# Kernel tuning notes

Measured on AMD Instinct MI355X. Metric: run time of the kernel, lower is better.

The kernel has to match this reference:

```python
import jax, jax.numpy as jnp
import numpy as np

# Batched-graph geometry: 128 graphs x 400 nodes x 6400 edges
N_GRAPHS = 128
NODES_PER = 400
EDGES_PER = 6400
N_NODES = N_GRAPHS * NODES_PER      # 51200
N_EDGES = N_GRAPHS * EDGES_PER      # 819200
F_IN = 256
HID = 64
K = 8          # num_filtrations
D = 3          # outputs per coordinate function (4 funs -> 12 total)


def coord_feats(p, t_tri, t_gau, sig, W_lin, b_lin, c_rh, r_rh):
    """Apply the 4 coordinate transforms to persistence pairs p: [K, M, 2].
    Returns [M, K*4D] with layout cat-over-coordfuns inside, cat-over-filtrations outside,
    matching torch: cat([cat([mod(p_k) for mod in funs],1) for k],1)."""
    x0, x1 = p[..., 0:1], p[..., 1:2]                       # [K,M,1]
    tri = jax.nn.relu(x1 - jnp.abs(t_tri - x0))             # Triangle_transform -> [K,M,D]
    d2 = jnp.sum((p[..., None, :] - t_gau) ** 2, axis=-1)   # [K,M,D]
    gau = jnp.exp(-d2 / (2.0 * sig[0] ** 2))                # Gaussian_transform
    lin = p @ W_lin + b_lin                                 # Line_transform
    l1 = jnp.abs(x0 - c_rh) + jnp.abs(x1 - c_rh)            # L1 dist to centers
    rh = 1.0 / (1.0 + l1) - 1.0 / (1.0 + jnp.abs(jnp.abs(r_rh[0]) - l1))  # RationalHat
    feats = jnp.concatenate([tri, gau, lin, rh], axis=-1)   # [K,M,4D]
    Kk, M, Dd = feats.shape
    return feats.transpose(1, 0, 2).reshape(M, Kk * Dd)     # [M, K*4D]


def setup_inputs() -> dict:
    key = jax.random.key(0)
    ks = jax.random.split(key, 24)
    x = jax.random.normal(ks[0], (N_NODES, F_IN), jnp.float32)
    # edges drawn within each graph block
    offs = (jnp.arange(N_EDGES) // EDGES_PER) * NODES_PER
    edge_index = jax.random.randint(ks[1], (2, N_EDGES), 0, NODES_PER) + offs[None, :]
    batch_vec = jnp.arange(N_NODES) // NODES_PER            # graph id per node
    edge_slices = jnp.arange(N_GRAPHS + 1) * EDGES_PER
    s = lambda i, shape: (jax.random.normal(ks[i], shape, jnp.float32) * 0.1)
    inp = dict(
        x=x, edge_index=edge_index, batch_vec=batch_vec, edge_slices=edge_slices,
        # shared filtration MLP: Linear(F_IN,HID)-ReLU-Linear(HID,K)-ReLU
        W1=s(2, (F_IN, HID)), b1=jnp.zeros((HID,), jnp.float32),
        W2=s(3, (HID, K)), b2=jnp.zeros((K,), jnp.float32),
        # dim-0 coordinate-function params
        t_tri0=s(4, (D,)), t_gau0=s(5, (D, 2)), sig0=jnp.ones((1,), jnp.float32),
        W_lin0=s(6, (2, D)), b_lin0=jnp.zeros((D,), jnp.float32),
        c_rh0=s(7, (D,)), r_rh0=jnp.ones((1,), jnp.float32),
        # dim-1 coordinate-function params
        t_tri1=s(8, (D,)), t_gau1=s(9, (D, 2)), sig1=jnp.ones((1,), jnp.float32),
        W_lin1=s(10, (2, D)), b_lin1=jnp.zeros((D,), jnp.float32),
        c_rh1=s(11, (D,)), r_rh1=jnp.ones((1,), jnp.float32),
        # output linear: in = F_IN + 2*K*4D (dist_dim1=True, non-residual path)
        W_out=s(12, (F_IN + 2 * K * 4 * D, F_IN)), b_out=jnp.zeros((F_IN,), jnp.float32),
    )
    return inp


def reference(x, edge_index, batch_vec, edge_slices,
              W1, b1, W2, b2,
              t_tri0, t_gau0, sig0, W_lin0, b_lin0, c_rh0, r_rh0,
              t_tri1, t_gau1, sig1, W_lin1, b_lin1, c_rh1, r_rh1,
              W_out, b_out):
    # per-node filtration values (shared params, relu_filtrations)
    fv = jax.nn.relu(jax.nn.relu(x @ W1 + b1) @ W2 + b2)            # [N,K]
    # edge filtration = max of endpoint values
    fe = jnp.maximum(fv[edge_index[0]], fv[edge_index[1]])          # [E,K]
    # fake dim-0 persistence: pairs (v, v) for every vertex, per filtration
    pers0 = jnp.broadcast_to(fv.T[..., None], (K, fv.shape[0], 2))  # [K,N,2]
    # fake dim-1: one unpaired tuple per graph = max edge value, placed at first edge
    eb = batch_vec[edge_index[0]]                                   # [E] graph id per edge
    unpaired = jax.ops.segment_max(fe, eb, num_segments=N_GRAPHS)   # [B,K]
    chosen = edge_slices[:-1]                                       # deterministic edge per graph
    pers1 = jnp.zeros((edge_index.shape[1], K, 2), fv.dtype)
    pers1 = pers1.at[chosen, :, 0].set(unpaired)
    pers1 = pers1.transpose(1, 0, 2)                                # [K,E,2]
    # coordinate-function activations
    act0 = coord_feats(pers0, t_tri0, t_gau0, sig0, W_lin0, b_lin0, c_rh0, r_rh0)  # [N, K*12]
    mask = jnp.any(pers1 != 0, axis=(0, 2))                         # [E]
    act1 = coord_feats(pers1, t_tri1, t_gau1, sig1, W_lin1, b_lin1, c_rh1, r_rh1)  # [E, K*12]
    g1 = jax.ops.segment_sum(act1 * mask[:, None].astype(act1.dtype), eb,
                             num_segments=N_GRAPHS)                 # [B, K*12]
    concat = jnp.concatenate([x, act0, g1[batch_vec]], axis=1)      # [N, F_IN + 2*K*12]
    return jax.nn.relu(concat @ W_out + b_out)                      # [N, F_IN]
```

## Files before the change

kernel.cpp:

```cpp
#include <hip/hip_runtime.h>
#include <hip/hip_bf16.h>

#define N_GRAPHS 128
#define NODES_PER 400
#define EDGES_PER 6400
#define N_NODES (N_GRAPHS * NODES_PER)
#define N_EDGES (N_GRAPHS * EDGES_PER)
#define F_IN 256
#define HID 64
#define FEAT 96
#define KTOT 352

typedef __attribute__((ext_vector_type(8))) short bf16x8;
typedef __attribute__((ext_vector_type(4))) float f32x4;

union u4b8 { uint4 u; bf16x8 v; };

__device__ __forceinline__ unsigned short f2b(float f) {
  union { float f; unsigned int u; } c; c.f = f;
  const unsigned int r = c.u + 0x7FFFu + ((c.u >> 16) & 1u);
  return (unsigned short)(r >> 16);
}

__device__ __forceinline__ unsigned pkbf2(float lo, float hi) {
  __hip_bfloat162 h = __float22bfloat162_rn(make_float2(lo, hi));
  return *reinterpret_cast<unsigned*>(&h);
}

__device__ __forceinline__ float coord_one(
    int fun, int d, float x0, float x1,
    const float* __restrict__ t_tri, const float* __restrict__ t_gau,
    const float* __restrict__ sig, const float* __restrict__ W_lin,
    const float* __restrict__ b_lin, const float* __restrict__ c_rh,
    const float* __restrict__ r_rh) {
  if (fun == 0) {
    return fmaxf(x1 - fabsf(t_tri[d] - x0), 0.f);
  } else if (fun == 1) {
    const float dx = x0 - t_gau[d * 2 + 0];
    const float dy = x1 - t_gau[d * 2 + 1];
    const float s = sig[0];
    return expf(-(dx * dx + dy * dy) / (2.f * s * s));
  } else if (fun == 2) {
    return x0 * W_lin[d] + x1 * W_lin[3 + d] + b_lin[d];
  } else {
    const float l1 = fabsf(x0 - c_rh[d]) + fabsf(x1 - c_rh[d]);
    return 1.f / (1.f + l1) - 1.f / (1.f + fabsf(fabsf(r_rh[0]) - l1));
  }
}

__global__ __launch_bounds__(256) void k_wt(
    const float* __restrict__ W_out, const float* __restrict__ W1,
    unsigned short* __restrict__ Wt2, unsigned short* __restrict__ Wt1c) {
  const int idx = blockIdx.x * 256 + threadIdx.x;
  if (idx < KTOT * 256) {
    const int k = idx >> 8, c = idx & 255;
    Wt2[((size_t)(k >> 3) * 256 + c) * 8 + (k & 7)] = f2b(W_out[idx]);
  } else {
    const int j = idx - KTOT * 256;
    const int k = j >> 6, c = j & 63;
    Wt1c[((size_t)(k >> 3) * 64 + c) * 8 + (k & 7)] = f2b(W1[j]);
  }
}

__global__ __launch_bounds__(256, 3) void k_fv(
    const float* __restrict__ x, const unsigned short* __restrict__ Wt1c,
    const float* __restrict__ b1, const float* __restrict__ W2,
    const float* __restrict__ b2,
    const float* __restrict__ t_tri, const float* __restrict__ t_gau,
    const float* __restrict__ sig, const float* __restrict__ W_lin,
    const float* __restrict__ b_lin, const float* __restrict__ c_rh,
    const float* __restrict__ r_rh,
    float* __restrict__ fv, unsigned short* __restrict__ ext,
    unsigned short* __restrict__ xb, const int write_xb) {
  __shared__ float W2s[HID * 8];
  __shared__ float Hs[4][16][68];
  const int tid = threadIdx.x;
  const int wave = tid >> 6, lane = tid & 63;
  const int l15 = lane & 15, l4 = lane >> 4;
  const int n0 = blockIdx.x * 64;

  W2s[tid] = W2[tid];
  W2s[tid + 256] = W2[tid + 256];
  __syncthreads();

  const int arow = n0 + wave * 16 + l15;
  bf16x8 afr[8];
  #pragma unroll
  for (int kt = 0; kt < 8; ++kt) {
    const size_t go = (size_t)arow * F_IN + kt * 32 + l4 * 8;
    const float4 f0 = *(const float4*)&x[go];
    const float4 f1 = *(const float4*)&x[go + 4];
    u4b8 w;
    w.u.x = pkbf2(f0.x, f0.y);
    w.u.y = pkbf2(f0.z, f0.w);
    w.u.z = pkbf2(f1.x, f1.y);
    w.u.w = pkbf2(f1.z, f1.w);
    if (write_xb) *(uint4*)&xb[go] = w.u;
    afr[kt] = w.v;
  }

  f32x4 acc[4];
  #pragma unroll
  for (int nf = 0; nf < 4; ++nf) acc[nf] = (f32x4){0.f, 0.f, 0.f, 0.f};
  #pragma unroll
  for (int kt = 0; kt < 8; ++kt) {
    const unsigned short* wb = Wt1c + (size_t)(kt * 4 + l4) * 512;
    #pragma unroll
    for (int nf = 0; nf < 4; ++nf) {
      const bf16x8 b = *(const bf16x8*)&wb[(nf * 16 + l15) * 8];
      acc[nf] = __builtin_amdgcn_mfma_f32_16x16x32_bf16(afr[kt], b, acc[nf], 0, 0, 0);
    }
  }

  #pragma unroll
  for (int nf = 0; nf < 4; ++nf) {
    const int col = nf * 16 + l15;
    const float bb = b1[col];
    #pragma unroll
    for (int j = 0; j < 4; ++j)
      Hs[wave][l4 * 4 + j][col] = fmaxf(acc[nf][j] + bb, 0.f);
  }
  __syncthreads();

  #pragma unroll
  for (int p = tid; p < 512; p += 256) {
    const int row = p >> 3, kk = p & 7;
    const float* hr = Hs[row >> 4][row & 15];
    float s = b2[kk];
    #pragma unroll 8
    for (int j = 0; j < HID; ++j) s = fmaf(hr[j], W2s[j * 8 + kk], s);
    s = fmaxf(s, 0.f);
    const int n = n0 + row;
    fv[(size_t)n * 8 + kk] = s;

    float fo[12];
    #pragma unroll
    for (int fun = 0; fun < 4; ++fun)
      #pragma unroll
      for (int d = 0; d < 3; ++d)
        fo[fun * 3 + d] = coord_one(fun, d, s, s,
                                    t_tri, t_gau, sig, W_lin, b_lin, c_rh, r_rh);
    unsigned o32[6];
    #pragma unroll
    for (int i = 0; i < 6; ++i) o32[i] = pkbf2(fo[2 * i], fo[2 * i + 1]);
    unsigned short* dst = &ext[(size_t)n * FEAT + kk * 12];
    *(uint2*)&dst[0] = make_uint2(o32[0], o32[1]);
    *(uint2*)&dst[4] = make_uint2(o32[2], o32[3]);
    *(uint2*)&dst[8] = make_uint2(o32[4], o32[5]);
  }
}

#define CHUNK (EDGES_PER / 8)
__global__ __launch_bounds__(256) void k_unpaired(
    const int* __restrict__ ei, const float* __restrict__ fv,
    float* __restrict__ unpP) {
  __shared__ float lfv[NODES_PER * 8];
  __shared__ float red[256][8];
  const int g = blockIdx.x >> 3, ch = blockIdx.x & 7;
  const int tid = threadIdx.x;

  for (int i = tid; i < NODES_PER * 2; i += 256)
    *(float4*)&lfv[i * 4] = *(const float4*)&fv[(size_t)g * NODES_PER * 8 + i * 4];
  __syncthreads();

  float lm[8];
  #pragma unroll
  for (int k = 0; k < 8; ++k) lm[k] = 0.f;
  const int e0 = g * EDGES_PER + ch * CHUNK;
  for (int e = e0 + tid; e < e0 + CHUNK; e += 256) {
    const int a = ei[e] - g * NODES_PER;
    const int b = ei[N_EDGES + e] - g * NODES_PER;
    const float4 a0 = *(const float4*)&lfv[a * 8];
    const float4 a1 = *(const float4*)&lfv[a * 8 + 4];
    const float4 b0 = *(const float4*)&lfv[b * 8];
    const float4 b1 = *(const float4*)&lfv[b * 8 + 4];
    lm[0] = fmaxf(lm[0], fmaxf(a0.x, b0.x));
    lm[1] = fmaxf(lm[1], fmaxf(a0.y, b0.y));
    lm[2] = fmaxf(lm[2], fmaxf(a0.z, b0.z));
    lm[3] = fmaxf(lm[3], fmaxf(a0.w, b0.w));
    lm[4] = fmaxf(lm[4], fmaxf(a1.x, b1.x));
    lm[5] = fmaxf(lm[5], fmaxf(a1.y, b1.y));
    lm[6] = fmaxf(lm[6], fmaxf(a1.z, b1.z));
    lm[7] = fmaxf(lm[7], fmaxf(a1.w, b1.w));
  }
  #pragma unroll
  for (int k = 0; k < 8; ++k) red[tid][k] = lm[k];
  __syncthreads();
  for (int s = 128; s > 0; s >>= 1) {
    if (tid < s) {
      #pragma unroll
      for (int k = 0; k < 8; ++k)
        red[tid][k] = fmaxf(red[tid][k], red[tid + s][k]);
    }
    __syncthreads();
  }
  if (tid < 8) unpP[(size_t)(g * 8 + ch) * 8 + tid] = red[0][tid];
}

__global__ __launch_bounds__(256) void k_g1G(
    const float* __restrict__ unpP, const float* __restrict__ t_tri,
    const float* __restrict__ t_gau, const float* __restrict__ sig,
    const float* __restrict__ W_lin, const float* __restrict__ b_lin,
    const float* __restrict__ c_rh, const float* __restrict__ r_rh,
    const float* __restrict__ W_out, const float* __restrict__ b_out,
    float* __restrict__ G) {
  const int g = blockIdx.x;
  const int t = threadIdx.x;
  __shared__ float u[8];
  __shared__ float feat[96];
  if (t < 8) {
    float m = 0.f;
    #pragma unroll
    for (int ch = 0; ch < 8; ++ch)
      m = fmaxf(m, unpP[(size_t)(g * 8 + ch) * 8 + t]);
    u[t] = m;
  }
  __syncthreads();
  if (t < 96) {
    const float mask = (u[0] != 0.f || u[1] != 0.f || u[2] != 0.f ||
                        u[3] != 0.f || u[4] != 0.f || u[5] != 0.f ||
                        u[6] != 0.f || u[7] != 0.f) ? 1.f : 0.f;
    const int k = t / 12;
    const int fun = (t % 12) / 3;
    const int d = t % 3;
    feat[t] = mask * coord_one(fun, d, u[k], 0.f,
                               t_tri, t_gau, sig, W_lin, b_lin, c_rh, r_rh);
  }
  __syncthreads();
  float s = b_out[t];
  #pragma unroll 4
  for (int f = 0; f < 96; ++f)
    s = fmaf(feat[f], W_out[(size_t)(352 + f) * 256 + t], s);
  G[g * 256 + t] = s;
}

__global__ __launch_bounds__(512, 4) void k_out_mfma(
    const float* __restrict__ x, const unsigned short* __restrict__ xb,
    const unsigned short* __restrict__ ext,
    const unsigned short* __restrict__ Wt2, const float* __restrict__ G,
    float* __restrict__ out, const int use_xb) {
  const int tid = threadIdx.x;
  const int wave = tid >> 6, lane = tid & 63;
  const int l15 = lane & 15, l4 = lane >> 4;
  const int c0 = wave * 32;

  bf16x8 b[11][2];
  #pragma unroll
  for (int ks = 0; ks < 11; ++ks)
    #pragma unroll
    for (int nf = 0; nf < 2; ++nf)
      b[ks][nf] = *(const bf16x8*)
          &Wt2[((size_t)(ks * 4 + l4) * 256 + c0 + nf * 16 + l15) * 8];

  for (int t = blockIdx.x; t < N_NODES / 16; t += gridDim.x) {
    const int arow = t * 16 + l15;
    const int gidx = t / 25;

    f32x4 acc[2];
    acc[0] = (f32x4){0.f, 0.f, 0.f, 0.f};
    acc[1] = (f32x4){0.f, 0.f, 0.f, 0.f};

    if (use_xb) {
      #pragma unroll
      for (int ks = 0; ks < 11; ++ks) {
        const bf16x8 a = (ks < 8)
            ? *(const bf16x8*)&xb[(size_t)arow * F_IN + ks * 32 + l4 * 8]
            : *(const bf16x8*)&ext[(size_t)arow * FEAT + (ks - 8) * 32 + l4 * 8];
        acc[0] = __builtin_amdgcn_mfma_f32_16x16x32_bf16(a, b[ks][0], acc[0], 0, 0, 0);
        acc[1] = __builtin_amdgcn_mfma_f32_16x16x32_bf16(a, b[ks][1], acc[1], 0, 0, 0);
      }
    } else {
      #pragma unroll
      for (int ks = 0; ks < 11; ++ks) {
        bf16x8 a;
        if (ks < 8) {
          const size_t go = (size_t)arow * F_IN + ks * 32 + l4 * 8;
          const float4 f0 = *(const float4*)&x[go];
          const float4 f1 = *(const float4*)&x[go + 4];
          u4b8 w;
          w.u.x = pkbf2(f0.x, f0.y);
          w.u.y = pkbf2(f0.z, f0.w);
          w.u.z = pkbf2(f1.x, f1.y);
          w.u.w = pkbf2(f1.z, f1.w);
          a = w.v;
        } else {
          a = *(const bf16x8*)&ext[(size_t)arow * FEAT + (ks - 8) * 32 + l4 * 8];
        }
        acc[0] = __builtin_amdgcn_mfma_f32_16x16x32_bf16(a, b[ks][0], acc[0], 0, 0, 0);
        acc[1] = __builtin_amdgcn_mfma_f32_16x16x32_bf16(a, b[ks][1], acc[1], 0, 0, 0);
      }
    }

    #pragma unroll
    for (int nf = 0; nf < 2; ++nf) {
      const int col = c0 + nf * 16 + l15;
      const float gv = G[gidx * 256 + col];
      #pragma unroll
      for (int j = 0; j < 4; ++j) {
        const int row = t * 16 + l4 * 4 + j;
        out[(size_t)row * 256 + col] = fmaxf(acc[nf][j] + gv, 0.f);
      }
    }
  }
}

extern "C" void kernel_launch(void* const* d_in, const int* in_sizes, int n_in,
                              void* d_out, int out_size, void* d_ws, size_t ws_size,
                              hipStream_t stream) {
  const float* x          = (const float*)d_in[0];
  const int*   edge_index = (const int*)d_in[1];
  const float* W1     = (const float*)d_in[4];
  const float* b1     = (const float*)d_in[5];
  const float* W2     = (const float*)d_in[6];
  const float* b2     = (const float*)d_in[7];
  const float* t_tri0 = (const float*)d_in[8];
  const float* t_gau0 = (const float*)d_in[9];
  const float* sig0   = (const float*)d_in[10];
  const float* W_lin0 = (const float*)d_in[11];
  const float* b_lin0 = (const float*)d_in[12];
  const float* c_rh0  = (const float*)d_in[13];
  const float* r_rh0  = (const float*)d_in[14];
  const float* t_tri1 = (const float*)d_in[15];
  const float* t_gau1 = (const float*)d_in[16];
  const float* sig1   = (const float*)d_in[17];
  const float* W_lin1 = (const float*)d_in[18];
  const float* b_lin1 = (const float*)d_in[19];
  const float* c_rh1  = (const float*)d_in[20];
  const float* r_rh1  = (const float*)d_in[21];
  const float* W_out  = (const float*)d_in[22];
  const float* b_out  = (const float*)d_in[23];
  float* out = (float*)d_out;

  char* base = (char*)d_ws;
  float* fv            = (float*)(base + 0);
  float* unpP          = (float*)(base + 1638400);
  float* G             = (float*)(base + 1671168);
  unsigned short* Wt2  = (unsigned short*)(base + 1802240);
  unsigned short* Wt1c = (unsigned short*)(base + 1982464);
  unsigned short* ext  = (unsigned short*)(base + 2015232);
  unsigned short* xb   = (unsigned short*)(base + 11845632);
  const size_t ws_need_xb = 11845632 + (size_t)N_NODES * F_IN * 2;
  const int use_xb = ws_size >= ws_need_xb ? 1 : 0;

  k_wt<<<(KTOT * 256 + F_IN * HID) / 256, 256, 0, stream>>>(W_out, W1, Wt2, Wt1c);
  k_fv<<<N_NODES / 64, 256, 0, stream>>>(
      x, Wt1c, b1, W2, b2,
      t_tri0, t_gau0, sig0, W_lin0, b_lin0, c_rh0, r_rh0,
      fv, ext, xb, use_xb);
  k_unpaired<<<N_GRAPHS * 8, 256, 0, stream>>>(edge_index, fv, unpP);
  k_g1G<<<N_GRAPHS, 256, 0, stream>>>(unpP, t_tri1, t_gau1, sig1,
                                      W_lin1, b_lin1, c_rh1, r_rh1,
                                      W_out, b_out, G);
  k_out_mfma<<<512, 512, 0, stream>>>(x, xb, ext, Wt2, G, out, use_xb);
}
```

Baseline: 86.23 us.

## Stage output-GEMM weights in LDS and split columns across blocks

The final output GEMM kernel now copies a 64-column slice of the bf16 weight matrix into shared memory once per block, instead of holding 22 weight fragments in registers per wave. Each wave computes a full 16x64 tile: A fragments are loaded once into registers and reused across 4 column groups, with B read from LDS. The grid becomes 768 blocks of 256 threads, each block owning one column quarter. This cuts register pressure and redundant A-row loads, at the cost of LDS traffic and four blocks each re-reading the same A rows.

```diff
diff --git a/kernel.cpp b/kernel.cpp
--- a/kernel.cpp
+++ b/kernel.cpp
@@ -234,65 +234,69 @@
   G[g * 256 + t] = s;
 }
 
-__global__ __launch_bounds__(512, 4) void k_out_mfma(
+__global__ __launch_bounds__(256, 3) void k_out_mfma(
     const float* __restrict__ x, const unsigned short* __restrict__ xb,
     const unsigned short* __restrict__ ext,
     const unsigned short* __restrict__ Wt2, const float* __restrict__ G,
     float* __restrict__ out, const int use_xb) {
+  __shared__ unsigned short Bs[44 * 64 * 8];
   const int tid = threadIdx.x;
   const int wave = tid >> 6, lane = tid & 63;
   const int l15 = lane & 15, l4 = lane >> 4;
-  const int c0 = wave * 32;
-
-  bf16x8 b[11][2];
-  #pragma unroll
-  for (int ks = 0; ks < 11; ++ks)
-    #pragma unroll
-    for (int nf = 0; nf < 2; ++nf)
-      b[ks][nf] = *(const bf16x8*)
-          &Wt2[((size_t)(ks * 4 + l4) * 256 + c0 + nf * 16 + l15) * 8];
-
-  for (int t = blockIdx.x; t < N_NODES / 16; t += gridDim.x) {
+  const int fam = blockIdx.x & 3;
+  const int bgrp = blockIdx.x >> 2;
+  const int c0 = fam * 64;
+
+  for (int c = tid; c < 44 * 64; c += 256) {
+    const int kk = c >> 6, col = c & 63;
+    *(uint4*)&Bs[(size_t)c * 8] =
+        *(const uint4*)&Wt2[((size_t)kk * 256 + c0 + col) * 8];
+  }
+  __syncthreads();
+
+  for (int t = bgrp * 4 + wave; t < N_NODES / 16; t += 768) {
+    asm volatile("" ::: "memory");
     const int arow = t * 16 + l15;
     const int gidx = t / 25;
 
-    f32x4 acc[2];
-    acc[0] = (f32x4){0.f, 0.f, 0.f, 0.f};
-    acc[1] = (f32x4){0.f, 0.f, 0.f, 0.f};
-
+    bf16x8 a[11];
     if (use_xb) {
       #pragma unroll
-      for (int ks = 0; ks < 11; ++ks) {
-        const bf16x8 a = (ks < 8)
-            ? *(const bf16x8*)&xb[(size_t)arow * F_IN + ks * 32 + l4 * 8]
-            : *(const bf16x8*)&ext[(size_t)arow * FEAT + (ks - 8) * 32 + l4 * 8];
-        acc[0] = __builtin_amdgcn_mfma_f32_16x16x32_bf16(a, b[ks][0], acc[0], 0, 0, 0);
-        acc[1] = __builtin_amdgcn_mfma_f32_16x16x32_bf16(a, b[ks][1], acc[1], 0, 0, 0);
+      for (int ks = 0; ks < 8; ++ks)
+        a[ks] = *(const bf16x8*)&xb[(size_t)arow * F_IN + ks * 32 + l4 * 8];
+    } else {
+      #pragma unroll
+      for (int ks = 0; ks < 8; ++ks) {
+        const size_t go = (size_t)arow * F_IN + ks * 32 + l4 * 8;
+        const float4 f0 = *(const float4*)&x[go];
+        const float4 f1 = *(const float4*)&x[go + 4];
+        u4b8 w;
+        w.u.x = pkbf2(f0.x, f0.y);
+        w.u.y = pkbf2(f0.z, f0.w);
+        w.u.z = pkbf2(f1.x, f1.y);
+        w.u.w = pkbf2(f1.z, f1.w);
+        a[ks] = w.v;
       }
-    } else {
-      #pragma unroll
-      for (int ks = 0; ks < 11; ++ks) {
-        bf16x8 a;
-        if (ks < 8) {
-          const size_t go = (size_t)arow * F_IN + ks * 32 + l4 * 8;
-          const float4 f0 = *(const float4*)&x[go];
-          const float4 f1 = *(const float4*)&x[go + 4];
-          u4b8 w;
-          w.u.x = pkbf2(f0.x, f0.y);
-          w.u.y = pkbf2(f0.z, f0.w);
-          w.u.z = pkbf2(f1.x, f1.y);
-          w.u.w = pkbf2(f1.z, f1.w);
-          a = w.v;
-        } else {
-          a = *(const bf16x8*)&ext[(size_t)arow * FEAT + (ks - 8) * 32 + l4 * 8];
-        }
-        acc[0] = __builtin_amdgcn_mfma_f32_16x16x32_bf16(a, b[ks][0], acc[0], 0, 0, 0);
-        acc[1] = __builtin_amdgcn_mfma_f32_16x16x32_bf16(a, b[ks][1], acc[1], 0, 0, 0);
+    }
+    #pragma unroll
+    for (int ks = 8; ks < 11; ++ks)
+      a[ks] = *(const bf16x8*)&ext[(size_t)arow * FEAT + (ks - 8) * 32 + l4 * 8];
+
+    f32x4 acc[4];
+    #pragma unroll
+    for (int nf = 0; nf < 4; ++nf) acc[nf] = (f32x4){0.f, 0.f, 0.f, 0.f};
+    #pragma unroll
+    for (int ks = 0; ks < 11; ++ks) {
+      const int kk = ks * 4 + l4;
+      #pragma unroll
+      for (int nf = 0; nf < 4; ++nf) {
+        const bf16x8 b = *(const bf16x8*)&Bs[((size_t)kk * 64 + nf * 16 + l15) * 8];
+        acc[nf] = __builtin_amdgcn_mfma_f32_16x16x32_bf16(a[ks], b, acc[nf], 0, 0, 0);
       }
     }
 
     #pragma unroll
-    for (int nf = 0; nf < 2; ++nf) {
+    for (int nf = 0; nf < 4; ++nf) {
       const int col = c0 + nf * 16 + l15;
       const float gv = G[gidx * 256 + col];
       #pragma unroll
@@ -351,5 +355,5 @@
   k_g1G<<<N_GRAPHS, 256, 0, stream>>>(unpP, t_tri1, t_gau1, sig1,
                                       W_lin1, b_lin1, c_rh1, r_rh1,
                                       W_out, b_out, G);
-  k_out_mfma<<<512, 512, 0, stream>>>(x, xb, ext, Wt2, G, out, use_xb);
-}
+  k_out_mfma<<<768, 256, 0, stream>>>(x, xb, ext, Wt2, G, out, use_xb);
+}
```

New measurement: 82.13 us. -4.8%, faster.
